# Performance work log

Hardware: AMD Instinct MI355X
Metric: run time of the kernel (lower is better)

## Reference

```python
import jax, jax.numpy as jnp
import numpy as np

N = 256        # num_nodes
F = 256        # feature_dim
B = 32         # batch
DEG = 32       # out-degree per node -> E = N*DEG edges


def setup_inputs() -> dict:
    key = jax.random.key(0)
    k1, k2, k3, k4 = jax.random.split(key, 4)
    node_features = jax.random.normal(k1, (B, N, F), dtype=jnp.float32)
    # xavier_uniform for [N, N, F] tensor: fan_in = N*F, fan_out = N*F per torch default flattening
    limit = float(np.sqrt(6.0 / (N * F + N * F)))
    W = jax.random.uniform(k2, (N, N, F), dtype=jnp.float32, minval=-limit, maxval=limit)
    phase = jax.random.uniform(k3, (N, N), dtype=jnp.float32, minval=0.0, maxval=2.0 * np.pi)
    # topology: each node i has DEG outgoing connections (paths[i])
    src = jnp.repeat(jnp.arange(N, dtype=jnp.int64), DEG)              # [E]
    dst = jax.random.randint(k4, (N * DEG,), 0, N, dtype=jnp.int64)    # [E]
    return {"node_features": node_features, "W": W, "phase": phase, "src": src, "dst": dst}


def reference(node_features, W, phase, src, dst):
    # real(exp(i*phase)) == cos(phase); per-edge effective weight [E, F]
    eff_w = W[src, dst, :] * jnp.cos(phase[src, dst])[:, None]
    # gather source node features and scale: [B, E, F]
    signal = node_features[:, src, :] * eff_w[None, :, :]
    # scatter-add into destination nodes
    propagated = jnp.zeros_like(node_features).at[:, dst, :].add(signal)
    # normalization by out-degree of each node index (matches original indexing)
    n = node_features.shape[1]
    counts = jnp.zeros((n,), dtype=node_features.dtype).at[src].add(1.0)
    norm = jnp.maximum(counts, 1.0)
    return propagated / norm[None, :, None]
```

## Files before the change

kernel.cpp:

```cpp
#include <hip/hip_runtime.h>
#include <math.h>

#define NN 256
#define FF 256
#define BB 32
#define EE 8192
#define F4  (FF / 4)
#define NF4 (NN * F4)


#define CAP 64

__global__ __launch_bounds__(1024, 4) void fused_propagate_kernel(
    const float4* __restrict__ nf4,
    const float4* __restrict__ W4,
    const float*  __restrict__ phase,
    const int*    __restrict__ dst,
    float4*       __restrict__ out4)
{
    const int d    = blockIdx.x;
    const int t    = threadIdx.x;
    const int lane = t & 63;
    const int wv   = t >> 6;

    __shared__ int          scnt[NN];
    __shared__ unsigned int s_pk[CAP / 4];
    __shared__ float        a_list[CAP];
    __shared__ int          wtot[4];
    __shared__ float4       aw4[CAP * 64];

    const int4* dstq = (const int4*)dst;
    const int4 v0 = dstq[t];
    const int4 v1 = dstq[t + 1024];
    int c0 = (v0.x == d) + (v0.y == d) + (v0.z == d) + (v0.w == d);
    int c1 = (v1.x == d) + (v1.y == d) + (v1.z == d) + (v1.w == d);
    #pragma unroll
    for (int off = 1; off < 8; off <<= 1) {
        c0 += __shfl_xor(c0, off, 64);
        c1 += __shfl_xor(c1, off, 64);
    }
    if ((t & 7) == 0) {
        scnt[t >> 3]         = c0;
        scnt[128 + (t >> 3)] = c1;
    }
    __syncthreads();

    int cnt = 0, ind = 0;
    if (t < NN) { cnt = scnt[t]; ind = (cnt > 0) ? 1 : 0; }

    const unsigned long long mask  = __ballot(ind);
    const int                below = __popcll(mask & ((1ULL << lane) - 1ULL));
    if (wv < 4 && lane == 0) wtot[wv] = __popcll(mask);
    __syncthreads();

    const int total = wtot[0] + wtot[1] + wtot[2] + wtot[3];
    int wbase = 0;
    #pragma unroll
    for (int w = 0; w < 4; w++) wbase += (w < wv) ? wtot[w] : 0;

    unsigned char* s8w = (unsigned char*)s_pk;
    if (ind) {
        const float a = (float)cnt * cosf(phase[t * NN + d]) * 0.03125f;
        const int pos = wbase + below;
        s8w[pos]    = (unsigned char)t;
        a_list[pos] = a;
    }
    const int n4 = (total + 3) & ~3;
    if (t < n4 - total) {
        s8w[total + t]    = 0;
        a_list[total + t] = 0.0f;
    }
    __syncthreads();

    const int q  = t & 63;
    const int bg = t >> 6;
    const float4* nfa = nf4 + bg * NF4 + q;
    const float4* nfb = nf4 + (bg + 16) * NF4 + q;

    float4 xa0, xa1, xa2, xa3, xb0, xb1, xb2, xb3;
    {
        const unsigned int su = s_pk[0];
        const int sA = (int)(su & 255u), sB = (int)((su >> 8) & 255u);
        const int sC = (int)((su >> 16) & 255u), sD = (int)(su >> 24);
        xa0 = nfa[sA * 64]; xb0 = nfb[sA * 64];
        xa1 = nfa[sB * 64]; xb1 = nfb[sB * 64];
        xa2 = nfa[sC * 64]; xb2 = nfb[sC * 64];
        xa3 = nfa[sD * 64]; xb3 = nfb[sD * 64];
    }

    const int drow = d * F4;
    const unsigned char* s8 = (const unsigned char*)s_pk;
    for (int slot = t; slot < (n4 << 6); slot += 1024) {
        const int   e = slot >> 6, f = slot & 63;
        const float a = a_list[e];
        float4 w = W4[(int)s8[e] * NF4 + drow + f];
        w.x *= a; w.y *= a; w.z *= a; w.w *= a;
        aw4[slot] = w;
    }
    __syncthreads();

    float4 acc0 = {0.f, 0.f, 0.f, 0.f};
    float4 acc1 = {0.f, 0.f, 0.f, 0.f};

    if (n4 > 0) {
        for (int k = 4; k < n4; k += 4) {
            const unsigned int sn = s_pk[k >> 2];
            const int sE = (int)(sn & 255u), sF = (int)((sn >> 8) & 255u);
            const int sG = (int)((sn >> 16) & 255u), sH = (int)(sn >> 24);
            const float4 ya0 = nfa[sE * 64], yb0 = nfb[sE * 64];
            const float4 ya1 = nfa[sF * 64], yb1 = nfb[sF * 64];
            const float4 ya2 = nfa[sG * 64], yb2 = nfb[sG * 64];
            const float4 ya3 = nfa[sH * 64], yb3 = nfb[sH * 64];

            {
                const float4 a0 = aw4[(k - 4) * 64 + q];
                const float4 a1 = aw4[(k - 3) * 64 + q];
                const float4 a2 = aw4[(k - 2) * 64 + q];
                const float4 a3 = aw4[(k - 1) * 64 + q];
                acc0.x = fmaf(xa0.x, a0.x, acc0.x); acc0.y = fmaf(xa0.y, a0.y, acc0.y);
                acc0.z = fmaf(xa0.z, a0.z, acc0.z); acc0.w = fmaf(xa0.w, a0.w, acc0.w);
                acc1.x = fmaf(xb0.x, a0.x, acc1.x); acc1.y = fmaf(xb0.y, a0.y, acc1.y);
                acc1.z = fmaf(xb0.z, a0.z, acc1.z); acc1.w = fmaf(xb0.w, a0.w, acc1.w);
                acc0.x = fmaf(xa1.x, a1.x, acc0.x); acc0.y = fmaf(xa1.y, a1.y, acc0.y);
                acc0.z = fmaf(xa1.z, a1.z, acc0.z); acc0.w = fmaf(xa1.w, a1.w, acc0.w);
                acc1.x = fmaf(xb1.x, a1.x, acc1.x); acc1.y = fmaf(xb1.y, a1.y, acc1.y);
                acc1.z = fmaf(xb1.z, a1.z, acc1.z); acc1.w = fmaf(xb1.w, a1.w, acc1.w);
                acc0.x = fmaf(xa2.x, a2.x, acc0.x); acc0.y = fmaf(xa2.y, a2.y, acc0.y);
                acc0.z = fmaf(xa2.z, a2.z, acc0.z); acc0.w = fmaf(xa2.w, a2.w, acc0.w);
                acc1.x = fmaf(xb2.x, a2.x, acc1.x); acc1.y = fmaf(xb2.y, a2.y, acc1.y);
                acc1.z = fmaf(xb2.z, a2.z, acc1.z); acc1.w = fmaf(xb2.w, a2.w, acc1.w);
                acc0.x = fmaf(xa3.x, a3.x, acc0.x); acc0.y = fmaf(xa3.y, a3.y, acc0.y);
                acc0.z = fmaf(xa3.z, a3.z, acc0.z); acc0.w = fmaf(xa3.w, a3.w, acc0.w);
                acc1.x = fmaf(xb3.x, a3.x, acc1.x); acc1.y = fmaf(xb3.y, a3.y, acc1.y);
                acc1.z = fmaf(xb3.z, a3.z, acc1.z); acc1.w = fmaf(xb3.w, a3.w, acc1.w);
            }
            xa0 = ya0; xa1 = ya1; xa2 = ya2; xa3 = ya3;
            xb0 = yb0; xb1 = yb1; xb2 = yb2; xb3 = yb3;
        }

        {
            const float4 a0 = aw4[(n4 - 4) * 64 + q];
            const float4 a1 = aw4[(n4 - 3) * 64 + q];
            const float4 a2 = aw4[(n4 - 2) * 64 + q];
            const float4 a3 = aw4[(n4 - 1) * 64 + q];
            acc0.x = fmaf(xa0.x, a0.x, acc0.x); acc0.y = fmaf(xa0.y, a0.y, acc0.y);
            acc0.z = fmaf(xa0.z, a0.z, acc0.z); acc0.w = fmaf(xa0.w, a0.w, acc0.w);
            acc1.x = fmaf(xb0.x, a0.x, acc1.x); acc1.y = fmaf(xb0.y, a0.y, acc1.y);
            acc1.z = fmaf(xb0.z, a0.z, acc1.z); acc1.w = fmaf(xb0.w, a0.w, acc1.w);
            acc0.x = fmaf(xa1.x, a1.x, acc0.x); acc0.y = fmaf(xa1.y, a1.y, acc0.y);
            acc0.z = fmaf(xa1.z, a1.z, acc0.z); acc0.w = fmaf(xa1.w, a1.w, acc0.w);
            acc1.x = fmaf(xb1.x, a1.x, acc1.x); acc1.y = fmaf(xb1.y, a1.y, acc1.y);
            acc1.z = fmaf(xb1.z, a1.z, acc1.z); acc1.w = fmaf(xb1.w, a1.w, acc1.w);
            acc0.x = fmaf(xa2.x, a2.x, acc0.x); acc0.y = fmaf(xa2.y, a2.y, acc0.y);
            acc0.z = fmaf(xa2.z, a2.z, acc0.z); acc0.w = fmaf(xa2.w, a2.w, acc0.w);
            acc1.x = fmaf(xb2.x, a2.x, acc1.x); acc1.y = fmaf(xb2.y, a2.y, acc1.y);
            acc1.z = fmaf(xb2.z, a2.z, acc1.z); acc1.w = fmaf(xb2.w, a2.w, acc1.w);
            acc0.x = fmaf(xa3.x, a3.x, acc0.x); acc0.y = fmaf(xa3.y, a3.y, acc0.y);
            acc0.z = fmaf(xa3.z, a3.z, acc0.z); acc0.w = fmaf(xa3.w, a3.w, acc0.w);
            acc1.x = fmaf(xb3.x, a3.x, acc1.x); acc1.y = fmaf(xb3.y, a3.y, acc1.y);
            acc1.z = fmaf(xb3.z, a3.z, acc1.z); acc1.w = fmaf(xb3.w, a3.w, acc1.w);
        }
    }

    out4[bg * NF4 + drow + q]        = acc0;
    out4[(bg + 16) * NF4 + drow + q] = acc1;
}

extern "C" void kernel_launch(void* const* d_in, const int* in_sizes, int n_in,
                              void* d_out, int out_size, void* d_ws, size_t ws_size,
                              hipStream_t stream) {
    const float* nf    = (const float*)d_in[0];
    const float* W     = (const float*)d_in[1];
    const float* phase = (const float*)d_in[2];
    const int*   dst   = (const int*)d_in[4];
    float*       out   = (float*)d_out;

    fused_propagate_kernel<<<NN, 1024, 0, stream>>>(
        (const float4*)nf, (const float4*)W, phase, dst, (float4*)out);
}
```

Measured before the change: 114.6 us.

## Split fused propagate into prep and gather kernels via workspace

Splits the single fused kernel into two launches. A prep kernel builds, per destination node, the compacted source list and the scaled weight rows, and writes them to the workspace. A gather kernel then runs 4x more blocks of 512 threads, each handling 8 batches, reading the weights from global memory instead of shared memory. This is meant to raise parallelism and occupancy, since the old kernel used large shared memory and 1024-thread blocks. The cost is an extra launch and a round trip of the weights through global memory, and the fused kernel stays as a fallback when the workspace is too small.

```diff
diff --git a/kernel.cpp b/kernel.cpp
--- a/kernel.cpp
+++ b/kernel.cpp
@@ -11,12 +11,13 @@
 
 #define CAP 64
 
-__global__ __launch_bounds__(1024, 4) void fused_propagate_kernel(
-    const float4* __restrict__ nf4,
+__global__ __launch_bounds__(256, 4) void prep_kernel(
     const float4* __restrict__ W4,
     const float*  __restrict__ phase,
     const int*    __restrict__ dst,
-    float4*       __restrict__ out4)
+    float4*       __restrict__ aw_ws,
+    int*          __restrict__ n4_arr,
+    unsigned int* __restrict__ spk_arr)
 {
     const int d    = blockIdx.x;
     const int t    = threadIdx.x;
@@ -27,30 +28,32 @@
     __shared__ unsigned int s_pk[CAP / 4];
     __shared__ float        a_list[CAP];
     __shared__ int          wtot[4];
-    __shared__ float4       aw4[CAP * 64];
 
     const int4* dstq = (const int4*)dst;
-    const int4 v0 = dstq[t];
-    const int4 v1 = dstq[t + 1024];
-    int c0 = (v0.x == d) + (v0.y == d) + (v0.z == d) + (v0.w == d);
-    int c1 = (v1.x == d) + (v1.y == d) + (v1.z == d) + (v1.w == d);
+    int c[8];
+    #pragma unroll
+    for (int i = 0; i < 8; i++) {
+        const int4 v = dstq[t + 256 * i];
+        c[i] = (v.x == d) + (v.y == d) + (v.z == d) + (v.w == d);
+    }
     #pragma unroll
     for (int off = 1; off < 8; off <<= 1) {
-        c0 += __shfl_xor(c0, off, 64);
-        c1 += __shfl_xor(c1, off, 64);
+        #pragma unroll
+        for (int i = 0; i < 8; i++) c[i] += __shfl_xor(c[i], off, 64);
     }
     if ((t & 7) == 0) {
-        scnt[t >> 3]         = c0;
-        scnt[128 + (t >> 3)] = c1;
-    }
-    __syncthreads();
-
-    int cnt = 0, ind = 0;
-    if (t < NN) { cnt = scnt[t]; ind = (cnt > 0) ? 1 : 0; }
+        const int g = t >> 3;
+        #pragma unroll
+        for (int i = 0; i < 8; i++) scnt[g + 32 * i] = c[i];
+    }
+    __syncthreads();
+
+    const int cnt = scnt[t];
+    const int ind = (cnt > 0) ? 1 : 0;
 
     const unsigned long long mask  = __ballot(ind);
     const int                below = __popcll(mask & ((1ULL << lane) - 1ULL));
-    if (wv < 4 && lane == 0) wtot[wv] = __popcll(mask);
+    if (lane == 0) wtot[wv] = __popcll(mask);
     __syncthreads();
 
     const int total = wtot[0] + wtot[1] + wtot[2] + wtot[3];
@@ -72,11 +75,144 @@
     }
     __syncthreads();
 
+    if (t == 0)  n4_arr[d] = n4;
+    if (t < 16)  spk_arr[d * 16 + t] = s_pk[t];
+
+    const int drow = d * F4;
+    const unsigned char* s8 = (const unsigned char*)s_pk;
+    float4* awd = aw_ws + d * (CAP * 64);
+    for (int slot = t; slot < (n4 << 6); slot += 256) {
+        const int   e = slot >> 6, f = slot & 63;
+        const float a = a_list[e];
+        float4 w = W4[(int)s8[e] * NF4 + drow + f];
+        w.x *= a; w.y *= a; w.z *= a; w.w *= a;
+        awd[slot] = w;
+    }
+}
+
+__global__ __launch_bounds__(512, 4) void gather_kernel(
+    const float4*       __restrict__ nf4,
+    const float4*       __restrict__ aw_ws,
+    const int*          __restrict__ n4_arr,
+    const unsigned int* __restrict__ spk_arr,
+    float4*             __restrict__ out4)
+{
+    const int bid = blockIdx.x;
+    const int d   = bid >> 2;
+    const int bq  = bid & 3;
+    const int t   = threadIdx.x;
+    const int q   = t & 63;
+    const int b   = bq * 8 + (t >> 6);
+
+    __shared__ unsigned int spk_l[16];
+    __shared__ int          n4s;
+    if (t < 16) spk_l[t] = spk_arr[d * 16 + t];
+    if (t == 0) n4s = n4_arr[d];
+    __syncthreads();
+    const int n4 = n4s;
+
+    const float4* awd = aw_ws + d * (CAP * 64) + q;
+    const float4* nfp = nf4 + b * NF4 + q;
+
+    float4 acc = {0.f, 0.f, 0.f, 0.f};
+
+    if (n4 > 0) {
+        const unsigned int su = spk_l[0];
+        const int s0 = (int)(su & 255u), s1 = (int)((su >> 8) & 255u);
+        const int s2 = (int)((su >> 16) & 255u), s3 = (int)(su >> 24);
+        float4 a0 = awd[0 * 64], a1 = awd[1 * 64];
+        float4 a2 = awd[2 * 64], a3 = awd[3 * 64];
+        float4 x0 = nfp[s0 * 64], x1 = nfp[s1 * 64];
+        float4 x2 = nfp[s2 * 64], x3 = nfp[s3 * 64];
+
+        for (int k = 4; k < n4; k += 4) {
+            const unsigned int sn = spk_l[k >> 2];
+            const int sE = (int)(sn & 255u), sF = (int)((sn >> 8) & 255u);
+            const int sG = (int)((sn >> 16) & 255u), sH = (int)(sn >> 24);
+            const float4 an0 = awd[(k + 0) * 64], an1 = awd[(k + 1) * 64];
+            const float4 an2 = awd[(k + 2) * 64], an3 = awd[(k + 3) * 64];
+            const float4 y0 = nfp[sE * 64], y1 = nfp[sF * 64];
+            const float4 y2 = nfp[sG * 64], y3 = nfp[sH * 64];
+
+            acc.x = fmaf(x0.x, a0.x, acc.x); acc.y = fmaf(x0.y, a0.y, acc.y);
+            acc.z = fmaf(x0.z, a0.z, acc.z); acc.w = fmaf(x0.w, a0.w, acc.w);
+            acc.x = fmaf(x1.x, a1.x, acc.x); acc.y = fmaf(x1.y, a1.y, acc.y);
+            acc.z = fmaf(x1.z, a1.z, acc.z); acc.w = fmaf(x1.w, a1.w, acc.w);
+            acc.x = fmaf(x2.x, a2.x, acc.x); acc.y = fmaf(x2.y, a2.y, acc.y);
+            acc.z = fmaf(x2.z, a2.z, acc.z); acc.w = fmaf(x2.w, a2.w, acc.w);
+            acc.x = fmaf(x3.x, a3.x, acc.x); acc.y = fmaf(x3.y, a3.y, acc.y);
+            acc.z = fmaf(x3.z, a3.z, acc.z); acc.w = fmaf(x3.w, a3.w, acc.w);
+
+            a0 = an0; a1 = an1; a2 = an2; a3 = an3;
+            x0 = y0;  x1 = y1;  x2 = y2;  x3 = y3;
+        }
+
+        acc.x = fmaf(x0.x, a0.x, acc.x); acc.y = fmaf(x0.y, a0.y, acc.y);
+        acc.z = fmaf(x0.z, a0.z, acc.z); acc.w = fmaf(x0.w, a0.w, acc.w);
+        acc.x = fmaf(x1.x, a1.x, acc.x); acc.y = fmaf(x1.y, a1.y, acc.y);
+        acc.z = fmaf(x1.z, a1.z, acc.z); acc.w = fmaf(x1.w, a1.w, acc.w);
+        acc.x = fmaf(x2.x, a2.x, acc.x); acc.y = fmaf(x2.y, a2.y, acc.y);
+        acc.z = fmaf(x2.z, a2.z, acc.z); acc.w = fmaf(x2.w, a2.w, acc.w);
+        acc.x = fmaf(x3.x, a3.x, acc.x); acc.y = fmaf(x3.y, a3.y, acc.y);
+        acc.z = fmaf(x3.z, a3.z, acc.z); acc.w = fmaf(x3.w, a3.w, acc.w);
+    }
+
+    out4[b * NF4 + d * F4 + q] = acc;
+}
+
+__global__ __launch_bounds__(1024, 4) void fused_propagate_kernel(
+    const float4* __restrict__ nf4, const float4* __restrict__ W4,
+    const float* __restrict__ phase, const int* __restrict__ dst,
+    float4* __restrict__ out4)
+{
+    const int d    = blockIdx.x;
+    const int t    = threadIdx.x;
+    const int lane = t & 63;
+    const int wv   = t >> 6;
+
+    __shared__ int          scnt[NN];
+    __shared__ unsigned int s_pk[CAP / 4];
+    __shared__ float        a_list[CAP];
+    __shared__ int          wtot[4];
+    __shared__ float4       aw4[CAP * 64];
+
+    const int4* dstq = (const int4*)dst;
+    const int4 v0 = dstq[t];
+    const int4 v1 = dstq[t + 1024];
+    int c0 = (v0.x == d) + (v0.y == d) + (v0.z == d) + (v0.w == d);
+    int c1 = (v1.x == d) + (v1.y == d) + (v1.z == d) + (v1.w == d);
+    #pragma unroll
+    for (int off = 1; off < 8; off <<= 1) {
+        c0 += __shfl_xor(c0, off, 64);
+        c1 += __shfl_xor(c1, off, 64);
+    }
+    if ((t & 7) == 0) { scnt[t >> 3] = c0; scnt[128 + (t >> 3)] = c1; }
+    __syncthreads();
+
+    int cnt = 0, ind = 0;
+    if (t < NN) { cnt = scnt[t]; ind = (cnt > 0) ? 1 : 0; }
+    const unsigned long long mask  = __ballot(ind);
+    const int                below = __popcll(mask & ((1ULL << lane) - 1ULL));
+    if (wv < 4 && lane == 0) wtot[wv] = __popcll(mask);
+    __syncthreads();
+    const int total = wtot[0] + wtot[1] + wtot[2] + wtot[3];
+    int wbase = 0;
+    #pragma unroll
+    for (int w = 0; w < 4; w++) wbase += (w < wv) ? wtot[w] : 0;
+    unsigned char* s8w = (unsigned char*)s_pk;
+    if (ind) {
+        const float a = (float)cnt * cosf(phase[t * NN + d]) * 0.03125f;
+        const int pos = wbase + below;
+        s8w[pos] = (unsigned char)t; a_list[pos] = a;
+    }
+    const int n4 = (total + 3) & ~3;
+    if (t < n4 - total) { s8w[total + t] = 0; a_list[total + t] = 0.0f; }
+    __syncthreads();
+
     const int q  = t & 63;
     const int bg = t >> 6;
     const float4* nfa = nf4 + bg * NF4 + q;
     const float4* nfb = nf4 + (bg + 16) * NF4 + q;
-
     float4 xa0, xa1, xa2, xa3, xb0, xb1, xb2, xb3;
     {
         const unsigned int su = s_pk[0];
@@ -87,11 +223,10 @@
         xa2 = nfa[sC * 64]; xb2 = nfb[sC * 64];
         xa3 = nfa[sD * 64]; xb3 = nfb[sD * 64];
     }
-
     const int drow = d * F4;
     const unsigned char* s8 = (const unsigned char*)s_pk;
     for (int slot = t; slot < (n4 << 6); slot += 1024) {
-        const int   e = slot >> 6, f = slot & 63;
+        const int e = slot >> 6, f = slot & 63;
         const float a = a_list[e];
         float4 w = W4[(int)s8[e] * NF4 + drow + f];
         w.x *= a; w.y *= a; w.z *= a; w.w *= a;
@@ -101,7 +236,6 @@
 
     float4 acc0 = {0.f, 0.f, 0.f, 0.f};
     float4 acc1 = {0.f, 0.f, 0.f, 0.f};
-
     if (n4 > 0) {
         for (int k = 4; k < n4; k += 4) {
             const unsigned int sn = s_pk[k >> 2];
@@ -111,7 +245,6 @@
             const float4 ya1 = nfa[sF * 64], yb1 = nfb[sF * 64];
             const float4 ya2 = nfa[sG * 64], yb2 = nfb[sG * 64];
             const float4 ya3 = nfa[sH * 64], yb3 = nfb[sH * 64];
-
             {
                 const float4 a0 = aw4[(k - 4) * 64 + q];
                 const float4 a1 = aw4[(k - 3) * 64 + q];
@@ -137,7 +270,6 @@
             xa0 = ya0; xa1 = ya1; xa2 = ya2; xa3 = ya3;
             xb0 = yb0; xb1 = yb1; xb2 = yb2; xb3 = yb3;
         }
-
         {
             const float4 a0 = aw4[(n4 - 4) * 64 + q];
             const float4 a1 = aw4[(n4 - 3) * 64 + q];
@@ -161,7 +293,6 @@
             acc1.z = fmaf(xb3.z, a3.z, acc1.z); acc1.w = fmaf(xb3.w, a3.w, acc1.w);
         }
     }
-
     out4[bg * NF4 + drow + q]        = acc0;
     out4[(bg + 16) * NF4 + drow + q] = acc1;
 }
@@ -175,6 +306,20 @@
     const int*   dst   = (const int*)d_in[4];
     float*       out   = (float*)d_out;
 
-    fused_propagate_kernel<<<NN, 1024, 0, stream>>>(
-        (const float4*)nf, (const float4*)W, phase, dst, (float4*)out);
+    const size_t aw_bytes = (size_t)NN * CAP * 64 * sizeof(float4);
+    const size_t need     = aw_bytes + NN * sizeof(int) + NN * 16 * sizeof(unsigned int);
+
+    if (d_ws != nullptr && ws_size >= need) {
+        float4*       aw_ws   = (float4*)d_ws;
+        int*          n4_arr  = (int*)((char*)d_ws + aw_bytes);
+        unsigned int* spk_arr = (unsigned int*)((char*)d_ws + aw_bytes + NN * sizeof(int));
+
+        prep_kernel<<<NN, 256, 0, stream>>>(
+            (const float4*)W, phase, dst, aw_ws, n4_arr, spk_arr);
+        gather_kernel<<<NN * 4, 512, 0, stream>>>(
+            (const float4*)nf, aw_ws, n4_arr, spk_arr, (float4*)out);
+    } else {
+        fused_propagate_kernel<<<NN, 1024, 0, stream>>>(
+            (const float4*)nf, (const float4*)W, phase, dst, (float4*)out);
+    }
 }
```

After: 129.9 us. +13.3%, slower.
